# Performance work log

Hardware: AMD Instinct MI355X
Metric: run time of the kernel (lower is better)

Reference implementation:

```python
import jax, jax.numpy as jnp
import numpy as np

HIDDEN = 4096
N_HEADS = 32
N_KV_HEADS = 8
HEAD_DIM = HIDDEN // N_HEADS  # 128
N_REP = N_HEADS // N_KV_HEADS  # 4
ROPE_THETA = 10000.0
B, S = 2, 2048


def setup_inputs() -> dict:
    key = jax.random.key(0)
    ks = jax.random.split(key, 9)
    sc = 1.0 / np.sqrt(HIDDEN)
    query = jax.random.normal(ks[0], (B, S, HIDDEN), jnp.float32)
    key_t = jax.random.normal(ks[1], (B, S, HIDDEN), jnp.float32)
    value = jax.random.normal(ks[2], (B, S, HIDDEN), jnp.float32)
    position_ids = jnp.sort(jax.random.randint(ks[3], (B, S), 0, S), axis=-1)
    Wq = jax.random.normal(ks[4], (HIDDEN, N_HEADS * HEAD_DIM), jnp.float32) * sc
    Wk = jax.random.normal(ks[5], (HIDDEN, N_KV_HEADS * HEAD_DIM), jnp.float32) * sc
    Wv = jax.random.normal(ks[6], (HIDDEN, N_KV_HEADS * HEAD_DIM), jnp.float32) * sc
    Wo = jax.random.normal(ks[7], (N_HEADS * HEAD_DIM, HIDDEN), jnp.float32) * sc
    return {"query": query, "key": key_t, "value": value,
            "position_ids": position_ids,
            "Wq": Wq, "Wk": Wk, "Wv": Wv, "Wo": Wo}


def _rotate_half(x):
    x1, x2 = jnp.split(x, 2, axis=-1)
    return jnp.concatenate((-x2, x1), axis=-1)


def _rope_cos_sin(position_ids):
    # inv_freq: [head_dim/2]
    inv_freq = 1.0 / (ROPE_THETA ** (jnp.arange(0, HEAD_DIM, 2, dtype=jnp.float32) / HEAD_DIM))
    # freqs: [B, S, head_dim/2] via per-position lookup (equiv. to cache gather cos_cached[position_ids])
    freqs = position_ids[..., None].astype(jnp.float32) * inv_freq
    emb = jnp.concatenate((freqs, freqs), axis=-1)          # [B, S, head_dim]
    return jnp.cos(emb)[:, None, :, :], jnp.sin(emb)[:, None, :, :]  # [B,1,S,hd]


def reference(query, key, value, position_ids, Wq, Wk, Wv, Wo):
    nb, q_len, _ = query.shape
    # QKV projections (bias-free linear)
    q = jnp.einsum('bse,ef->bsf', query, Wq).reshape(nb, q_len, N_HEADS, HEAD_DIM).transpose(0, 2, 1, 3)
    k = jnp.einsum('bse,ef->bsf', key, Wk).reshape(nb, q_len, N_KV_HEADS, HEAD_DIM).transpose(0, 2, 1, 3)
    v = jnp.einsum('bse,ef->bsf', value, Wv).reshape(nb, q_len, N_KV_HEADS, HEAD_DIM).transpose(0, 2, 1, 3)
    # RoPE
    cos, sin = _rope_cos_sin(position_ids)
    q = q * cos + _rotate_half(q) * sin
    k = k * cos + _rotate_half(k) * sin
    # GQA repeat_kv: [B, kvH, S, d] -> [B, H, S, d]
    k = jnp.repeat(k, N_REP, axis=1)
    v = jnp.repeat(v, N_REP, axis=1)
    # scaled dot-product attention (flash-attn semantics, no padding mask)
    scale = 1.0 / jnp.sqrt(jnp.asarray(HEAD_DIM, q.dtype))
    scores = jnp.einsum('bhqd,bhkd->bhqk', q, k) * scale
    probs = jax.nn.softmax(scores, axis=-1)
    ctx = jnp.einsum('bhqk,bhkd->bhqd', probs, v)
    ctx = ctx.transpose(0, 2, 1, 3).reshape(nb, q_len, N_HEADS * HEAD_DIM)
    return jnp.einsum('bsf,fe->bse', ctx, Wo)
```

## Files before the change

### kernel.cpp

```cpp
#include <hip/hip_runtime.h>
#include <hip/hip_bf16.h>

typedef __attribute__((ext_vector_type(8))) short bf16x8;
typedef __attribute__((ext_vector_type(4))) float f32x4;
typedef __attribute__((ext_vector_type(16))) float f32x16;
typedef __attribute__((ext_vector_type(2))) unsigned uint2x;

#define AS1(p) ((const __attribute__((address_space(1))) void*)(p))
#define AS3(p) ((__attribute__((address_space(3))) void*)(p))

__device__ inline unsigned cvtpk_bf16(float lo, float hi) {
  unsigned r;
  asm("v_cvt_pk_bf16_f32 %0, %1, %2" : "=v"(r) : "v"(lo), "v"(hi));
  return r;
}

__device__ inline uint2x plswap(unsigned a, unsigned b) {
  return __builtin_amdgcn_permlane32_swap(a, b, false, false);
}


__global__ __launch_bounds__(256) void xconv_kv(const float* __restrict__ k_in,
                                                const float* __restrict__ v_in,
                                                __hip_bfloat16* __restrict__ kc,
                                                __hip_bfloat16* __restrict__ vc) {
  const float* in = blockIdx.y ? v_in : k_in;
  __hip_bfloat16* out = blockIdx.y ? vc : kc;
  size_t i = ((size_t)blockIdx.x * 256 + threadIdx.x) * 4;
  float4 v = *(const float4*)(in + i);
  union { __hip_bfloat16 h[4]; ushort4 u; } o;
  o.h[0] = __float2bfloat16(v.x);
  o.h[1] = __float2bfloat16(v.y);
  o.h[2] = __float2bfloat16(v.z);
  o.h[3] = __float2bfloat16(v.w);
  *(ushort4*)(out + i) = o.u;
}

__global__ __launch_bounds__(256) void xconv(const float* __restrict__ in,
                                             __hip_bfloat16* __restrict__ out) {
  size_t i = ((size_t)blockIdx.x * 256 + threadIdx.x) * 4;
  float4 v = *(const float4*)(in + i);
  union { __hip_bfloat16 h[4]; ushort4 u; } o;
  o.h[0] = __float2bfloat16(v.x);
  o.h[1] = __float2bfloat16(v.y);
  o.h[2] = __float2bfloat16(v.z);
  o.h[3] = __float2bfloat16(v.w);
  *(ushort4*)(out + i) = o.u;
}

__global__ __launch_bounds__(256) void wtransAll(const float* __restrict__ Wq,
                                                 const float* __restrict__ Wo,
                                                 const float* __restrict__ Wk,
                                                 const float* __restrict__ Wv,
                                                 __hip_bfloat16* __restrict__ WqT,
                                                 __hip_bfloat16* __restrict__ WoT,
                                                 __hip_bfloat16* __restrict__ WkT,
                                                 __hip_bfloat16* __restrict__ WvT) {
  const int z = blockIdx.z;
  const int N = (z < 2) ? 4096 : 1024;
  const int n0 = blockIdx.x << 6;
  if (n0 >= N) return;
  const float* W = (z == 0) ? Wq : (z == 1) ? Wo : (z == 2) ? Wk : Wv;
  __hip_bfloat16* WT = (z == 0) ? WqT : (z == 1) ? WoT : (z == 2) ? WkT : WvT;
  __shared__ float t[64][68];
  const int k0 = blockIdx.y << 6;
  const int tx = threadIdx.x & 15, ty = threadIdx.x >> 4;
#pragma unroll
  for (int j = 0; j < 4; ++j) {
    const int k = ty + j * 16;
    float4 v = *(const float4*)(W + (size_t)(k0 + k) * N + n0 + tx * 4);
    t[tx * 4 + 0][k] = v.x;
    t[tx * 4 + 1][k] = v.y;
    t[tx * 4 + 2][k] = v.z;
    t[tx * 4 + 3][k] = v.w;
  }
  __syncthreads();
#pragma unroll
  for (int j = 0; j < 4; ++j) {
    const int n = ty + j * 16;
    float4 v = *(const float4*)(&t[n][tx * 4]);
    union { __hip_bfloat16 h[4]; ushort4 u; } o;
    o.h[0] = __float2bfloat16(v.x);
    o.h[1] = __float2bfloat16(v.y);
    o.h[2] = __float2bfloat16(v.z);
    o.h[3] = __float2bfloat16(v.w);
    *(ushort4*)(WT + (size_t)(n0 + n) * 4096 + k0 + tx * 4) = o.u;
  }
}

__global__ __launch_bounds__(256) void rope(__hip_bfloat16* __restrict__ X,
                                            const int* __restrict__ pos,
                                            int hbits, float scale) {
  const int t = blockIdx.x * 256 + threadIdx.x;
  const int j = t & 63;
  const int rest = t >> 6;
  const int h = rest & ((1 << hbits) - 1);
  const int row = rest >> hbits;
  const float p = (float)pos[row];
  const float fr = p * exp2f((float)j * -0.2076205059304601f);
  float sn, cs;
  __sincosf(fr, &sn, &cs);
  const size_t base = (((size_t)row << hbits) + h) * 128 + j;
  const float x0 = __bfloat162float(X[base]);
  const float x1 = __bfloat162float(X[base + 64]);
  X[base]      = __float2bfloat16((x0 * cs - x1 * sn) * scale);
  X[base + 64] = __float2bfloat16((x1 * cs + x0 * sn) * scale);
}


__device__ inline int tile_off(int row, int k) {
  return (((row >> 4) << 1) + (k >> 5)) * 512 + (row & 15) * 32 +
         ((k & 31) ^ ((row & 8) << 1));
}

__device__ inline void stageA(const __hip_bfloat16* __restrict__ src, int ld, int row0,
                              int kt, int h, __hip_bfloat16* ldsT, int w, int lane) {
#pragma unroll
  for (int li = 0; li < 2; ++li) {
    const int t = li * 8 + w;
    const int grp = ((t >> 3) << 1) + h;
    const int srl = (t & 7) >> 1, sk = t & 1;
    const int rowbase = grp * 64 + srl * 16;
    __hip_bfloat16* dst = ldsT + ((((rowbase >> 4) << 1) + sk) << 9);
    const int r = lane >> 2;
    const int ku = (lane & 3) ^ ((r & 8) >> 2);
    __builtin_amdgcn_global_load_lds(
        AS1(src + (size_t)(row0 + rowbase + r) * ld + kt + (sk << 5) + (ku << 3)),
        AS3(dst), 16, 0, 0);
  }
}

__device__ inline void stageB(const __hip_bfloat16* __restrict__ src, int ld, int col0,
                              int kt, int h, __hip_bfloat16* ldsT, int w, int lane) {
#pragma unroll
  for (int li = 0; li < 2; ++li) {
    const int t = li * 8 + w;
    const int q = t >> 2;
    const int srl = (t >> 1) & 1, sk = t & 1;
    const int colbase = q * 64 + h * 32 + srl * 16;
    __hip_bfloat16* dst = ldsT + ((((colbase >> 4) << 1) + sk) << 9);
    const int r = lane >> 2;
    const int ku = (lane & 3) ^ ((r & 8) >> 2);
    __builtin_amdgcn_global_load_lds(
        AS1(src + (size_t)(col0 + colbase + r) * ld + kt + (sk << 5) + (ku << 3)),
        AS3(dst), 16, 0, 0);
  }
}

template <int OUT_F32>
__global__ __launch_bounds__(512, 1) void gemm256(const __hip_bfloat16* __restrict__ A,
                                                  const __hip_bfloat16* __restrict__ BT,
                                                  void* __restrict__ Cout,
                                                  int M, int N, int K) {
  __shared__ __align__(16) __hip_bfloat16 lds[2][2][16384];
  const int tid = threadIdx.x;
  const int lane = tid & 63, w = tid >> 6;
  const int l15 = lane & 15, lg = lane >> 4;
  const int wm = w >> 2, wn = w & 3;
  const int nbx = N >> 8;
  const int nwg = (M >> 8) * nbx;
  const int bid = blockIdx.x;
  const int swz = (bid & 7) * (nwg >> 3) + (bid >> 3);
  const int m0 = (swz / nbx) << 8, n0 = (swz % nbx) << 8;

  f32x4 acc[8][4] = {};
  const int NT = K >> 6;

  stageA(A, K, m0, 0, 0, &lds[0][0][0], w, lane);
  stageB(BT, K, n0, 0, 0, &lds[0][1][0], w, lane);
  stageA(A, K, m0, 0, 1, &lds[0][0][0], w, lane);
  stageB(BT, K, n0, 0, 1, &lds[0][1][0], w, lane);
  stageA(A, K, m0, 64, 0, &lds[1][0][0], w, lane);
  stageB(BT, K, n0, 64, 0, &lds[1][1][0], w, lane);
  asm volatile("s_waitcnt vmcnt(4)" ::: "memory");
  __builtin_amdgcn_s_barrier();

  for (int j = 0; j < NT; ++j) {
    const int buf = j & 1;
    const __hip_bfloat16* Ab = &lds[buf][0][0];
    const __hip_bfloat16* Bb = &lds[buf][1][0];
    __hip_bfloat16* An = &lds[buf ^ 1][0][0];
    __hip_bfloat16* Bn = &lds[buf ^ 1][1][0];
    __hip_bfloat16* Ac = &lds[buf][0][0];
    __hip_bfloat16* Bc = &lds[buf][1][0];
    const int kt1 = (j + 1) << 6, kt2 = (j + 2) << 6;
    const bool s1 = (j + 1) < NT, s2 = (j + 2) < NT;

    auto phase = [&](int rq, int cq, int sid) {
      bf16x8 af[2][4], bfr[2][2];
#pragma unroll
      for (int kk = 0; kk < 2; ++kk) {
#pragma unroll
        for (int rf = 0; rf < 4; ++rf)
          af[kk][rf] = *(const bf16x8*)(Ab +
              tile_off(wm * 128 + (rq * 4 + rf) * 16 + l15, kk * 32 + lg * 8));
#pragma unroll
        for (int cf = 0; cf < 2; ++cf)
          bfr[kk][cf] = *(const bf16x8*)(Bb +
              tile_off(wn * 64 + (cq * 2 + cf) * 16 + l15, kk * 32 + lg * 8));
      }
      if (sid == 0)      { if (s1) stageA(A, K, m0, kt1, 1, An, w, lane); }
      else if (sid == 1) { if (s1) stageB(BT, K, n0, kt1, 1, Bn, w, lane); }
      else if (sid == 2) { if (s2) stageA(A, K, m0, kt2, 0, Ac, w, lane); }
      else {
        if (s2) stageB(BT, K, n0, kt2, 0, Bc, w, lane);
        if (s2) asm volatile("s_waitcnt vmcnt(4)" ::: "memory");
        else    asm volatile("s_waitcnt vmcnt(0)" ::: "memory");
      }
      __builtin_amdgcn_s_barrier();
      asm volatile("s_waitcnt lgkmcnt(0)" ::: "memory");
      __builtin_amdgcn_sched_barrier(0);
      __builtin_amdgcn_s_setprio(1);
#pragma unroll
      for (int kk = 0; kk < 2; ++kk)
#pragma unroll
        for (int rf = 0; rf < 4; ++rf)
#pragma unroll
          for (int cf = 0; cf < 2; ++cf)
            acc[rq * 4 + rf][cq * 2 + cf] = __builtin_amdgcn_mfma_f32_16x16x32_bf16(
                af[kk][rf], bfr[kk][cf], acc[rq * 4 + rf][cq * 2 + cf], 0, 0, 0);
      __builtin_amdgcn_s_setprio(0);
      __builtin_amdgcn_s_barrier();
    };
    phase(0, 0, 0);
    phase(0, 1, 1);
    phase(1, 0, 2);
    phase(1, 1, 3);
  }

#pragma unroll
  for (int rf = 0; rf < 8; ++rf)
#pragma unroll
    for (int cf = 0; cf < 4; ++cf)
#pragma unroll
      for (int i = 0; i < 4; ++i) {
        const size_t row = (size_t)(m0 + wm * 128 + rf * 16 + lg * 4 + i);
        const size_t col = (size_t)(n0 + wn * 64 + cf * 16 + l15);
        if (OUT_F32)
          ((float*)Cout)[row * N + col] = acc[rf][cf][i];
        else
          ((__hip_bfloat16*)Cout)[row * N + col] = __float2bfloat16(acc[rf][cf][i]);
      }
}

__global__ __launch_bounds__(512, 1) void gemm_kv8(const __hip_bfloat16* __restrict__ Ak,
                                                   const __hip_bfloat16* __restrict__ Av,
                                                   const __hip_bfloat16* __restrict__ BkT,
                                                   const __hip_bfloat16* __restrict__ BvT,
                                                   __hip_bfloat16* __restrict__ Kp,
                                                   __hip_bfloat16* __restrict__ VT) {
  __shared__ __align__(16) __hip_bfloat16 lds[2][24576];
  const int zz = blockIdx.z;
  const __hip_bfloat16* A  = zz ? Av : Ak;
  const __hip_bfloat16* BT = zz ? BvT : BkT;
  const int K = 4096;
  const int tid = threadIdx.x;
  const int lane = tid & 63, w = tid >> 6;
  const int l15 = lane & 15, lg = lane >> 4;
  const int wm = w >> 2, wn = w & 3;
  const int bid = blockIdx.x;
  const int swz = (bid & 7) * 16 + (bid >> 3);
  const int m0 = (swz >> 2) << 7;
  const int n0 = (swz & 3) << 8;

  auto stgA = [&](int kt, int h, __hip_bfloat16* ldsA) {
    const int r16 = 2 * h + ((w >> 2) << 2) + ((w >> 1) & 1);
    const int sk = w & 1;
    __hip_bfloat16* dst = ldsA + (((r16 << 1) + sk) << 9);
    const int r = lane >> 2;
    const int ku = (lane & 3) ^ ((r & 8) >> 2);
    __builtin_amdgcn_global_load_lds(
        AS1(A + (size_t)(m0 + r16 * 16 + r) * K + kt + (sk << 5) + (ku << 3)),
        AS3(dst), 16, 0, 0);
  };
  auto stgB = [&](int kt, int h, __hip_bfloat16* ldsB) {
#pragma unroll
    for (int li = 0; li < 2; ++li) {
      const int idx = li * 8 + w;
      const int r16 = ((idx >> 2) << 2) + 2 * h + ((idx >> 1) & 1);
      const int sk = idx & 1;
      __hip_bfloat16* dst = ldsB + (((r16 << 1) + sk) << 9);
      const int r = lane >> 2;
      const int ku = (lane & 3) ^ ((r & 8) >> 2);
      __builtin_amdgcn_global_load_lds(
          AS1(BT + (size_t)(n0 + r16 * 16 + r) * K + kt + (sk << 5) + (ku << 3)),
          AS3(dst), 16, 0, 0);
    }
  };

  f32x4 acc[4][4] = {};
  const int NT = K >> 6;

  stgA(0, 0, &lds[0][0]);
  stgB(0, 0, &lds[0][8192]);
  stgA(0, 1, &lds[0][0]);
  stgB(0, 1, &lds[0][8192]);
  stgA(64, 0, &lds[1][0]);
  stgB(64, 0, &lds[1][8192]);
  asm volatile("s_waitcnt vmcnt(3)" ::: "memory");
  __builtin_amdgcn_s_barrier();

  for (int j = 0; j < NT; ++j) {
    const int buf = j & 1;
    const __hip_bfloat16* Ab = &lds[buf][0];
    const __hip_bfloat16* Bb = &lds[buf][8192];
    __hip_bfloat16* An = &lds[buf ^ 1][0];
    __hip_bfloat16* Bn = &lds[buf ^ 1][8192];
    __hip_bfloat16* Ac = &lds[buf][0];
    __hip_bfloat16* Bc = &lds[buf][8192];
    const int kt1 = (j + 1) << 6, kt2 = (j + 2) << 6;
    const bool s1 = (j + 1) < NT, s2 = (j + 2) < NT;

    auto phase = [&](int rq, int cq, int sid) {
      bf16x8 af[2][2], bfr[2][2];
#pragma unroll
      for (int kk = 0; kk < 2; ++kk) {
#pragma unroll
        for (int rf = 0; rf < 2; ++rf)
          af[kk][rf] = *(const bf16x8*)(Ab +
              tile_off(wm * 64 + (rq * 2 + rf) * 16 + l15, kk * 32 + lg * 8));
#pragma unroll
        for (int cf = 0; cf < 2; ++cf)
          bfr[kk][cf] = *(const bf16x8*)(Bb +
              tile_off(wn * 64 + (cq * 2 + cf) * 16 + l15, kk * 32 + lg * 8));
      }
      if (sid == 0)      { if (s1) stgA(kt1, 1, An); }
      else if (sid == 1) { if (s1) stgB(kt1, 1, Bn); }
      else if (sid == 2) { if (s2) stgA(kt2, 0, Ac); }
      else {
        if (s2) stgB(kt2, 0, Bc);
        if (s2) asm volatile("s_waitcnt vmcnt(3)" ::: "memory");
        else    asm volatile("s_waitcnt vmcnt(0)" ::: "memory");
      }
      __builtin_amdgcn_s_barrier();
      asm volatile("s_waitcnt lgkmcnt(0)" ::: "memory");
      __builtin_amdgcn_sched_barrier(0);
      __builtin_amdgcn_s_setprio(1);
#pragma unroll
      for (int kk = 0; kk < 2; ++kk)
#pragma unroll
        for (int rf = 0; rf < 2; ++rf)
#pragma unroll
          for (int cf = 0; cf < 2; ++cf)
            acc[rq * 2 + rf][cq * 2 + cf] = __builtin_amdgcn_mfma_f32_16x16x32_bf16(
                af[kk][rf], bfr[kk][cf], acc[rq * 2 + rf][cq * 2 + cf], 0, 0, 0);
      __builtin_amdgcn_s_setprio(0);
      __builtin_amdgcn_s_barrier();
    };
    phase(0, 0, 0);
    phase(0, 1, 1);
    phase(1, 0, 2);
    phase(1, 1, 3);
  }

  if (zz == 0) {
#pragma unroll
    for (int rf = 0; rf < 4; ++rf)
#pragma unroll
      for (int cf = 0; cf < 4; ++cf)
#pragma unroll
        for (int i = 0; i < 4; ++i) {
          const size_t row = (size_t)(m0 + wm * 64 + rf * 16 + lg * 4 + i);
          const size_t col = (size_t)(n0 + wn * 64 + cf * 16 + l15);
          Kp[row * 1024 + col] = __float2bfloat16(acc[rf][cf][i]);
        }
  } else {
    const int b = m0 >> 11, s0g = m0 & 2047;
#pragma unroll
    for (int rf = 0; rf < 4; ++rf)
#pragma unroll
      for (int cf = 0; cf < 4; ++cf) {
        const int d = n0 + wn * 64 + cf * 16 + l15;
        const int g = d >> 7, dl = d & 127;
        const int srow = s0g + wm * 64 + rf * 16 + lg * 4;
        union { __hip_bfloat16 h[4]; unsigned long long u; } pkv;
#pragma unroll
        for (int i = 0; i < 4; ++i) pkv.h[i] = __float2bfloat16(acc[rf][cf][i]);
        *(unsigned long long*)(VT + ((size_t)(b * 8 + g) * 128 + dl) * 2048 + srow) = pkv.u;
      }
  }
}

__global__ __launch_bounds__(512) void attn(const __hip_bfloat16* __restrict__ Q,
                                            const __hip_bfloat16* __restrict__ Kp,
                                            const __hip_bfloat16* __restrict__ VT,
                                            const int* __restrict__ pos,
                                            __hip_bfloat16* __restrict__ ctx,
                                            float qs) {
  const int tid = threadIdx.x;
  const int lane = tid & 63, w = tid >> 6;
  const int l31 = lane & 31, hi = lane >> 5;
  const int qt = blockIdx.x, h = blockIdx.y, b = blockIdx.z;
  const int kvh = h >> 2;
  const int q0 = qt * 256 + w * 32;

  const __hip_bfloat16* Qh = Q + (size_t)(b * 2048) * 4096 + h * 128;
  const __hip_bfloat16* Kh = Kp + (size_t)(b * 2048) * 1024 + kvh * 128;
  const __hip_bfloat16* Vh = VT + (size_t)(b * 8 + kvh) * 128 * 2048;

  __shared__ __hip_bfloat16 Ks[2][64 * 128];
  __shared__ __hip_bfloat16 Vs[2][128 * 64];

  auto stage = [&](int buf, int s0) {
#pragma unroll
    for (int j = 0; j < 2; ++j) {
      const int idx = w * 64 + lane + j * 512;
      const int rK = idx >> 4, uK = idx & 15;
      __builtin_amdgcn_global_load_lds(
          AS1(Kh + (size_t)(s0 + rK) * 1024 + ((uK ^ (rK & 7)) << 3)),
          AS3(&Ks[buf][(w * 64 + j * 512) * 8]), 16, 0, 0);
      const int rV = idx >> 3, uV = idx & 7;
      __builtin_amdgcn_global_load_lds(
          AS1(Vh + (size_t)rV * 2048 + s0 + ((uV ^ (rV & 7)) << 3)),
          AS3(&Vs[buf][(w * 64 + j * 512) * 8]), 16, 0, 0);
    }
  };

  stage(0, 0);

  const int qrow = q0 + l31;
  const float pp = (float)pos[b * 2048 + qrow];
  bf16x8 qf[8];
  {
#pragma unroll
    for (int kd = 0; kd < 4; ++kd) {
      bf16x8 rlo = *(const bf16x8*)(Qh + (size_t)qrow * 4096 + kd * 16 + hi * 8);
      bf16x8 rhi = *(const bf16x8*)(Qh + (size_t)qrow * 4096 + (kd + 4) * 16 + hi * 8);
      bf16x8 olo, ohi;
#pragma unroll
      for (int e = 0; e < 8; ++e) {
        const int j = kd * 16 + hi * 8 + e;
        const float fr = pp * exp2f((float)j * -0.2076205059304601f);
        float sn, cs;
        __sincosf(fr, &sn, &cs);
        const float x0 = __uint_as_float(((unsigned)(unsigned short)rlo[e]) << 16);
        const float x1 = __uint_as_float(((unsigned)(unsigned short)rhi[e]) << 16);
        __hip_bfloat16 h0 = __float2bfloat16((x0 * cs - x1 * sn) * qs);
        __hip_bfloat16 h1 = __float2bfloat16((x1 * cs + x0 * sn) * qs);
        olo[e] = *(short*)&h0;
        ohi[e] = *(short*)&h1;
      }
      qf[kd] = olo;
      qf[kd + 4] = ohi;
    }
  }

  bf16x8 ones;
#pragma unroll
  for (int e = 0; e < 8; ++e) ones[e] = (short)0x3F80;

  f32x16 o[4] = {};
  f32x16 ol = {};
  __syncthreads();

  auto tile = [&](int tt, int cur, bool pf) {
    if (pf) stage(cur ^ 1, (tt + 1) * 64);

    f32x16 p[2] = {};
    __builtin_amdgcn_s_setprio(1);
#pragma unroll
    for (int n = 0; n < 2; ++n)
#pragma unroll
      for (int kd = 0; kd < 8; ++kd) {
        const int row = n * 32 + l31;
        bf16x8 kf = *(const bf16x8*)(&Ks[cur][row * 128 + (((2 * kd + hi) ^ (row & 7)) << 3)]);
        p[n] = __builtin_amdgcn_mfma_f32_32x32x16_bf16(kf, qf[kd], p[n], 0, 0, 0);
      }
    __builtin_amdgcn_s_setprio(0);

#pragma unroll
    for (int n = 0; n < 2; ++n)
#pragma unroll
      for (int e = 0; e < 16; ++e) p[n][e] = exp2f(p[n][e]);

    bf16x8 paf[4];
#pragma unroll
    for (int n = 0; n < 2; ++n)
#pragma unroll
      for (int ks = 0; ks < 2; ++ks) {
        const int bse = ks * 8;
        unsigned a1 = cvtpk_bf16(p[n][bse + 0], p[n][bse + 1]);
        unsigned b1 = cvtpk_bf16(p[n][bse + 4], p[n][bse + 5]);
        unsigned a2 = cvtpk_bf16(p[n][bse + 2], p[n][bse + 3]);
        unsigned b2 = cvtpk_bf16(p[n][bse + 6], p[n][bse + 7]);
        uint2x s1 = plswap(a1, b1);
        uint2x s2 = plswap(a2, b2);
        union { unsigned u[4]; bf16x8 v; } pw = {{s1[0], s2[0], s1[1], s2[1]}};
        paf[n * 2 + ks] = pw.v;
      }

    __builtin_amdgcn_s_setprio(1);
#pragma unroll
    for (int slot = 0; slot < 4; ++slot) {
      ol = __builtin_amdgcn_mfma_f32_32x32x16_bf16(ones, paf[slot], ol, 0, 0, 0);
#pragma unroll
      for (int dc = 0; dc < 4; ++dc) {
        const int row = dc * 32 + l31;
        bf16x8 vf = *(const bf16x8*)(&Vs[cur][row * 64 + (((2 * slot + hi) ^ (row & 7)) << 3)]);
        o[dc] = __builtin_amdgcn_mfma_f32_32x32x16_bf16(vf, paf[slot], o[dc], 0, 0, 0);
      }
    }
    __builtin_amdgcn_s_setprio(0);
    __syncthreads();
  };

  for (int t2 = 0; t2 < 16; ++t2) {
    tile(2 * t2, 0, true);
    tile(2 * t2 + 1, 1, t2 < 15);
  }

  const float inv = 1.0f / ol[0];
  const size_t rowbase = ((size_t)(b * 2048 + q0 + l31)) * 4096 + h * 128;
#pragma unroll
  for (int dc = 0; dc < 4; ++dc)
#pragma unroll
    for (int g = 0; g < 4; ++g) {
      union { unsigned short us[4]; ushort4 u4; } pk;
#pragma unroll
      for (int e = 0; e < 4; ++e) {
        __hip_bfloat16 hv = __float2bfloat16(o[dc][g * 4 + e] * inv);
        pk.us[e] = *(unsigned short*)&hv;
      }
      *(ushort4*)(ctx + rowbase + dc * 32 + g * 8 + hi * 4) = pk.u4;
    }
}


extern "C" void kernel_launch(void* const* d_in, const int* in_sizes, int n_in,
                              void* d_out, int out_size, void* d_ws, size_t ws_size,
                              hipStream_t stream) {
  const float* q_in = (const float*)d_in[0];
  const float* k_in = (const float*)d_in[1];
  const float* v_in = (const float*)d_in[2];
  const int* pos    = (const int*)d_in[3];
  const float* Wq   = (const float*)d_in[4];
  const float* Wk   = (const float*)d_in[5];
  const float* Wv   = (const float*)d_in[6];
  const float* Wo   = (const float*)d_in[7];

  char* ws = (char*)d_ws;
  __hip_bfloat16* xbuf = (__hip_bfloat16*)(ws);
  __hip_bfloat16* WqT  = (__hip_bfloat16*)(ws + 33554432);
  __hip_bfloat16* WkT  = (__hip_bfloat16*)(ws + 67108864);
  __hip_bfloat16* WvT  = (__hip_bfloat16*)(ws + 75497472);
  __hip_bfloat16* WoT  = (__hip_bfloat16*)(ws + 83886080);
  __hip_bfloat16* Qp   = (__hip_bfloat16*)(ws + 117440512);
  __hip_bfloat16* Kp   = (__hip_bfloat16*)(ws + 150994944);
  __hip_bfloat16* VTb  = (__hip_bfloat16*)(ws + 167772160);
  __hip_bfloat16* vconv = WqT;

  wtransAll<<<dim3(64, 64, 4), 256, 0, stream>>>(Wq, Wo, Wk, Wv, WqT, WoT, WkT, WvT);
  xconv<<<16384, 256, 0, stream>>>(q_in, xbuf);
  gemm256<0><<<256, 512, 0, stream>>>(xbuf, WqT, Qp, 4096, 4096, 4096);
  xconv_kv<<<dim3(16384, 2), 256, 0, stream>>>(k_in, v_in, xbuf, vconv);
  gemm_kv8<<<dim3(128, 1, 2), 512, 0, stream>>>(xbuf, vconv, WkT, WvT, Kp, VTb);
  rope<<<8192, 256, 0, stream>>>(Kp, pos, 3, 1.0f);
  attn<<<dim3(8, 32, 2), 512, 0, stream>>>(Qp, Kp, VTb, pos, xbuf,
                                           0.08838834764831845f * 1.4426950408889634f);
  gemm256<1><<<256, 512, 0, stream>>>(xbuf, WoT, d_out, 4096, 4096, 4096);
}
```

Baseline: 617.0 us.

## Fuse K RoPE into KV GEMM epilogue and merge weight/query prep kernels

Applies RoPE to K inside the gemm_kv8 epilogue. The accumulator tile is staged through LDS, then rotated and written with vectorized 16-byte stores, so the separate rope kernel's extra read and write pass over K goes away. The weight-transpose and query-conversion kernels are merged into one launch with five z-slices, removing a launch and letting the work overlap. The epilogue adds two block barriers and sincos work per element inside the GEMM.

```diff
diff --git a/kernel.cpp b/kernel.cpp
--- a/kernel.cpp
+++ b/kernel.cpp
@@ -19,6 +19,62 @@
   return __builtin_amdgcn_permlane32_swap(a, b, false, false);
 }
 
+__global__ __launch_bounds__(256) void prep(const float* __restrict__ Wq,
+                                            const float* __restrict__ Wo,
+                                            const float* __restrict__ Wk,
+                                            const float* __restrict__ Wv,
+                                            const float* __restrict__ q_in,
+                                            __hip_bfloat16* __restrict__ WqT,
+                                            __hip_bfloat16* __restrict__ WoT,
+                                            __hip_bfloat16* __restrict__ WkT,
+                                            __hip_bfloat16* __restrict__ WvT,
+                                            __hip_bfloat16* __restrict__ qc) {
+  const int z = blockIdx.z;
+  if (z == 4) {
+    const size_t b0 = (size_t)blockIdx.x * 4096;
+#pragma unroll
+    for (int c = 0; c < 4; ++c) {
+      const size_t i = b0 + c * 1024 + threadIdx.x * 4;
+      float4 v = *(const float4*)(q_in + i);
+      union { __hip_bfloat16 h[4]; ushort4 u; } o;
+      o.h[0] = __float2bfloat16(v.x);
+      o.h[1] = __float2bfloat16(v.y);
+      o.h[2] = __float2bfloat16(v.z);
+      o.h[3] = __float2bfloat16(v.w);
+      *(ushort4*)(qc + i) = o.u;
+    }
+    return;
+  }
+  const int N = (z < 2) ? 4096 : 1024;
+  const int n0 = (blockIdx.x & 63) << 6;
+  if (n0 >= N) return;
+  const int k0 = (blockIdx.x >> 6) << 6;
+  const float* W = (z == 0) ? Wq : (z == 1) ? Wo : (z == 2) ? Wk : Wv;
+  __hip_bfloat16* WT = (z == 0) ? WqT : (z == 1) ? WoT : (z == 2) ? WkT : WvT;
+  __shared__ float t[64][68];
+  const int tx = threadIdx.x & 15, ty = threadIdx.x >> 4;
+#pragma unroll
+  for (int j = 0; j < 4; ++j) {
+    const int k = ty + j * 16;
+    float4 v = *(const float4*)(W + (size_t)(k0 + k) * N + n0 + tx * 4);
+    t[tx * 4 + 0][k] = v.x;
+    t[tx * 4 + 1][k] = v.y;
+    t[tx * 4 + 2][k] = v.z;
+    t[tx * 4 + 3][k] = v.w;
+  }
+  __syncthreads();
+#pragma unroll
+  for (int j = 0; j < 4; ++j) {
+    const int n = ty + j * 16;
+    float4 v = *(const float4*)(&t[n][tx * 4]);
+    union { __hip_bfloat16 h[4]; ushort4 u; } o;
+    o.h[0] = __float2bfloat16(v.x);
+    o.h[1] = __float2bfloat16(v.y);
+    o.h[2] = __float2bfloat16(v.z);
+    o.h[3] = __float2bfloat16(v.w);
+    *(ushort4*)(WT + (size_t)(n0 + n) * 4096 + k0 + tx * 4) = o.u;
+  }
+}
 
 __global__ __launch_bounds__(256) void xconv_kv(const float* __restrict__ k_in,
                                                 const float* __restrict__ v_in,
@@ -34,77 +90,6 @@
   o.h[2] = __float2bfloat16(v.z);
   o.h[3] = __float2bfloat16(v.w);
   *(ushort4*)(out + i) = o.u;
-}
-
-__global__ __launch_bounds__(256) void xconv(const float* __restrict__ in,
-                                             __hip_bfloat16* __restrict__ out) {
-  size_t i = ((size_t)blockIdx.x * 256 + threadIdx.x) * 4;
-  float4 v = *(const float4*)(in + i);
-  union { __hip_bfloat16 h[4]; ushort4 u; } o;
-  o.h[0] = __float2bfloat16(v.x);
-  o.h[1] = __float2bfloat16(v.y);
-  o.h[2] = __float2bfloat16(v.z);
-  o.h[3] = __float2bfloat16(v.w);
-  *(ushort4*)(out + i) = o.u;
-}
-
-__global__ __launch_bounds__(256) void wtransAll(const float* __restrict__ Wq,
-                                                 const float* __restrict__ Wo,
-                                                 const float* __restrict__ Wk,
-                                                 const float* __restrict__ Wv,
-                                                 __hip_bfloat16* __restrict__ WqT,
-                                                 __hip_bfloat16* __restrict__ WoT,
-                                                 __hip_bfloat16* __restrict__ WkT,
-                                                 __hip_bfloat16* __restrict__ WvT) {
-  const int z = blockIdx.z;
-  const int N = (z < 2) ? 4096 : 1024;
-  const int n0 = blockIdx.x << 6;
-  if (n0 >= N) return;
-  const float* W = (z == 0) ? Wq : (z == 1) ? Wo : (z == 2) ? Wk : Wv;
-  __hip_bfloat16* WT = (z == 0) ? WqT : (z == 1) ? WoT : (z == 2) ? WkT : WvT;
-  __shared__ float t[64][68];
-  const int k0 = blockIdx.y << 6;
-  const int tx = threadIdx.x & 15, ty = threadIdx.x >> 4;
-#pragma unroll
-  for (int j = 0; j < 4; ++j) {
-    const int k = ty + j * 16;
-    float4 v = *(const float4*)(W + (size_t)(k0 + k) * N + n0 + tx * 4);
-    t[tx * 4 + 0][k] = v.x;
-    t[tx * 4 + 1][k] = v.y;
-    t[tx * 4 + 2][k] = v.z;
-    t[tx * 4 + 3][k] = v.w;
-  }
-  __syncthreads();
-#pragma unroll
-  for (int j = 0; j < 4; ++j) {
-    const int n = ty + j * 16;
-    float4 v = *(const float4*)(&t[n][tx * 4]);
-    union { __hip_bfloat16 h[4]; ushort4 u; } o;
-    o.h[0] = __float2bfloat16(v.x);
-    o.h[1] = __float2bfloat16(v.y);
-    o.h[2] = __float2bfloat16(v.z);
-    o.h[3] = __float2bfloat16(v.w);
-    *(ushort4*)(WT + (size_t)(n0 + n) * 4096 + k0 + tx * 4) = o.u;
-  }
-}
-
-__global__ __launch_bounds__(256) void rope(__hip_bfloat16* __restrict__ X,
-                                            const int* __restrict__ pos,
-                                            int hbits, float scale) {
-  const int t = blockIdx.x * 256 + threadIdx.x;
-  const int j = t & 63;
-  const int rest = t >> 6;
-  const int h = rest & ((1 << hbits) - 1);
-  const int row = rest >> hbits;
-  const float p = (float)pos[row];
-  const float fr = p * exp2f((float)j * -0.2076205059304601f);
-  float sn, cs;
-  __sincosf(fr, &sn, &cs);
-  const size_t base = (((size_t)row << hbits) + h) * 128 + j;
-  const float x0 = __bfloat162float(X[base]);
-  const float x1 = __bfloat162float(X[base + 64]);
-  X[base]      = __float2bfloat16((x0 * cs - x1 * sn) * scale);
-  X[base + 64] = __float2bfloat16((x1 * cs + x0 * sn) * scale);
 }
 
 
@@ -247,6 +232,7 @@
                                                    const __hip_bfloat16* __restrict__ Av,
                                                    const __hip_bfloat16* __restrict__ BkT,
                                                    const __hip_bfloat16* __restrict__ BvT,
+                                                   const int* __restrict__ pos,
                                                    __hip_bfloat16* __restrict__ Kp,
                                                    __hip_bfloat16* __restrict__ VT) {
   __shared__ __align__(16) __hip_bfloat16 lds[2][24576];
@@ -354,16 +340,42 @@
   }
 
   if (zz == 0) {
+    __syncthreads();
+    __hip_bfloat16* T = &lds[0][0];
+    const int TS = 264;
 #pragma unroll
     for (int rf = 0; rf < 4; ++rf)
 #pragma unroll
       for (int cf = 0; cf < 4; ++cf)
 #pragma unroll
-        for (int i = 0; i < 4; ++i) {
-          const size_t row = (size_t)(m0 + wm * 64 + rf * 16 + lg * 4 + i);
-          const size_t col = (size_t)(n0 + wn * 64 + cf * 16 + l15);
-          Kp[row * 1024 + col] = __float2bfloat16(acc[rf][cf][i]);
-        }
+        for (int i = 0; i < 4; ++i)
+          T[(wm * 64 + rf * 16 + lg * 4 + i) * TS + wn * 64 + cf * 16 + l15] =
+              __float2bfloat16(acc[rf][cf][i]);
+    __syncthreads();
+    const int row = tid >> 2, quad = tid & 3;
+    const int gr = m0 + row;
+    const float p = (float)pos[gr];
+#pragma unroll
+    for (int qb = 0; qb < 4; ++qb) {
+      const int bi = quad + qb * 4;
+      const int hl = bi >> 3, jb = (bi & 7) * 8;
+      bf16x8 lo  = *(const bf16x8*)&T[row * TS + hl * 128 + jb];
+      bf16x8 hi8 = *(const bf16x8*)&T[row * TS + hl * 128 + jb + 64];
+      union { __hip_bfloat16 h[8]; bf16x8 v; } o0, o1;
+#pragma unroll
+      for (int e = 0; e < 8; ++e) {
+        const int j = jb + e;
+        const float fr = p * exp2f((float)j * -0.2076205059304601f);
+        float sn, cs;
+        __sincosf(fr, &sn, &cs);
+        const float x0 = __uint_as_float(((unsigned)(unsigned short)lo[e]) << 16);
+        const float x1 = __uint_as_float(((unsigned)(unsigned short)hi8[e]) << 16);
+        o0.h[e] = __float2bfloat16(x0 * cs - x1 * sn);
+        o1.h[e] = __float2bfloat16(x1 * cs + x0 * sn);
+      }
+      *(bf16x8*)(Kp + (size_t)gr * 1024 + n0 + hl * 128 + jb)      = o0.v;
+      *(bf16x8*)(Kp + (size_t)gr * 1024 + n0 + hl * 128 + jb + 64) = o1.v;
+    }
   } else {
     const int b = m0 >> 11, s0g = m0 & 2047;
 #pragma unroll
@@ -549,12 +561,11 @@
   __hip_bfloat16* VTb  = (__hip_bfloat16*)(ws + 167772160);
   __hip_bfloat16* vconv = WqT;
 
-  wtransAll<<<dim3(64, 64, 4), 256, 0, stream>>>(Wq, Wo, Wk, Wv, WqT, WoT, WkT, WvT);
-  xconv<<<16384, 256, 0, stream>>>(q_in, xbuf);
+  prep<<<dim3(4096, 1, 5), 256, 0, stream>>>(Wq, Wo, Wk, Wv, q_in,
+                                             WqT, WoT, WkT, WvT, xbuf);
   gemm256<0><<<256, 512, 0, stream>>>(xbuf, WqT, Qp, 4096, 4096, 4096);
   xconv_kv<<<dim3(16384, 2), 256, 0, stream>>>(k_in, v_in, xbuf, vconv);
-  gemm_kv8<<<dim3(128, 1, 2), 512, 0, stream>>>(xbuf, vconv, WkT, WvT, Kp, VTb);
-  rope<<<8192, 256, 0, stream>>>(Kp, pos, 3, 1.0f);
+  gemm_kv8<<<dim3(128, 1, 2), 512, 0, stream>>>(xbuf, vconv, WkT, WvT, pos, Kp, VTb);
   attn<<<dim3(8, 32, 2), 512, 0, stream>>>(Qp, Kp, VTb, pos, xbuf,
                                            0.08838834764831845f * 1.4426950408889634f);
   gemm256<1><<<256, 512, 0, stream>>>(xbuf, WoT, d_out, 4096, 4096, 4096);
```

Measured after the change: 607.8 us. Within noise of the previous version (-1.5%).
